# Kernel tuning notes

Hardware: AMD Instinct MI355X
Metric: run time of the kernel (lower is better)

## Reference

```python
import jax, jax.numpy as jnp
import numpy as np

B, S, D, H = 2, 2048, 1024, 16
DK = D // H
WINDOW = 256


def _make_mask():
    # causal local-window sparsity: attend to j in (i-WINDOW, i]
    i = np.arange(S)[:, None]
    j = np.arange(S)[None, :]
    m = (j <= i) & (i - j < WINDOW)
    return jnp.asarray(m)


def setup_inputs() -> dict:
    key = jax.random.key(0)
    ks = jax.random.split(key, 9)
    sw = 1.0 / np.sqrt(D)
    return {
        "x": jax.random.normal(ks[0], (B, S, D), dtype=jnp.float32),
        "wq": jax.random.normal(ks[1], (D, D), dtype=jnp.float32) * sw,
        "bq": jnp.zeros((D,), dtype=jnp.float32),
        "wk": jax.random.normal(ks[2], (D, D), dtype=jnp.float32) * sw,
        "bk": jnp.zeros((D,), dtype=jnp.float32),
        "wv": jax.random.normal(ks[3], (D, D), dtype=jnp.float32) * sw,
        "bv": jnp.zeros((D,), dtype=jnp.float32),
        "wo": jax.random.normal(ks[4], (D, D), dtype=jnp.float32) * sw,
        "bo": jnp.zeros((D,), dtype=jnp.float32),
        "mask": _make_mask(),
    }


def reference(x, wq, bq, wk, bk, wv, bv, wo, bo, mask):
    b, s, d = x.shape
    # projections (torch Linear: x @ W.T + b), split heads -> [b, h, s, dk]
    def proj(w, bias):
        return (x @ w.T + bias).reshape(b, s, H, DK).transpose(0, 2, 1, 3)

    q = proj(wq, bq)
    k = proj(wk, bk)
    v = proj(wv, bv)

    scores = jnp.einsum("bhqd,bhkd->bhqk", q, k) / jnp.sqrt(jnp.float32(DK))
    scores = jnp.where(mask, scores, -jnp.inf)  # mask broadcasts over b, h
    attn = jax.nn.softmax(scores, axis=-1)
    out = jnp.einsum("bhqk,bhkd->bhqd", attn, v)
    out = out.transpose(0, 2, 1, 3).reshape(b, s, d)
    return out @ wo.T + bo
```

## Files before the change

### kernel.cpp

```cpp
#include <hip/hip_runtime.h>

#define S_LEN 2048
#define DMODEL 1024
#define NHEADS 16
#define WIN 256

typedef unsigned short u16;
typedef unsigned int u32;
typedef __attribute__((ext_vector_type(8))) __bf16 bf16x8;
typedef __attribute__((ext_vector_type(4))) float f32x4;
typedef __attribute__((ext_vector_type(8))) u16 u16x8;
typedef __attribute__((ext_vector_type(4))) u16 u16x4;

__device__ __forceinline__ u16 f2bf(float f) {
  u32 u = __builtin_bit_cast(u32, f);
  u += 0x7fffu + ((u >> 16) & 1u);
  return (u16)(u >> 16);
}

#define GLDS16(g, l) __builtin_amdgcn_global_load_lds( \
    (const __attribute__((address_space(1))) void*)(g), \
    (__attribute__((address_space(3))) void*)(l), 16, 0, 0)

__global__ __launch_bounds__(256) void cast_all(
    const float* __restrict__ x, const float* __restrict__ wq, const float* __restrict__ wk,
    const float* __restrict__ wv, const float* __restrict__ wo,
    u16* __restrict__ xb, u16* __restrict__ wqb, u16* __restrict__ wkb,
    u16* __restrict__ wvb, u16* __restrict__ wob) {
  const int e = (blockIdx.x * 256 + threadIdx.x) * 4;
  const float* src; u16* dst; int off;
  if (e < (1 << 22)) { src = x; dst = xb; off = e; }
  else {
    int r = e - (1 << 22);
    int seg = r >> 20; off = r & ((1 << 20) - 1);
    src = (seg == 0) ? wq : (seg == 1) ? wk : (seg == 2) ? wv : wo;
    dst = (seg == 0) ? wqb : (seg == 1) ? wkb : (seg == 2) ? wvb : wob;
  }
  float4 v = *(const float4*)(src + off);
  u16x4 o = { f2bf(v.x), f2bf(v.y), f2bf(v.z), f2bf(v.w) };
  *(u16x4*)(dst + off) = o;
}

__global__ __launch_bounds__(256) void gemm_nt(
    const u16* __restrict__ A,
    const u16* __restrict__ B0, const u16* __restrict__ B1, const u16* __restrict__ B2,
    const float* __restrict__ bias0, const float* __restrict__ bias1, const float* __restrict__ bias2,
    u16* __restrict__ C0, u16* __restrict__ C1, u16* __restrict__ C2,
    const int M, const int N, const int K)
{
  const u16* Bt; const float* bias; u16* C;
  if (blockIdx.z == 0)      { Bt = B0; bias = bias0; C = C0; }
  else if (blockIdx.z == 1) { Bt = B1; bias = bias1; C = C1; }
  else                      { Bt = B2; bias = bias2; C = C2; }

  __shared__ u16 As[2][128 * 32];
  __shared__ u16 Bs[2][128 * 32];

  const int t = threadIdx.x;
  const int row0 = blockIdx.x * 128;
  const int col0 = blockIdx.y * 128;
  const int lane = t & 63, lo = lane & 15, hi = lane >> 4;
  const int wv = t >> 6;
  const int wr = (wv >> 1) * 64, wc = (wv & 1) * 64;

  f32x4 acc[4][4];
  #pragma unroll
  for (int i = 0; i < 4; ++i)
    #pragma unroll
    for (int j = 0; j < 4; ++j) acc[i][j] = (f32x4)0.0f;

  const int NT = K >> 5;

  auto stage = [&](int buf, int kt) {
    const int kof = kt * 32;
    #pragma unroll
    for (int c = 0; c < 2; ++c) {
      const int off = t * 16 + c * 4096;
      const int r = off >> 6;
      const int ke = (off & 63) >> 1;
      GLDS16(A  + (size_t)(row0 + r) * K + (kof + ke), (u16*)As + buf * (128 * 32) + (off >> 1));
      GLDS16(Bt + (size_t)(col0 + r) * K + (kof + ke), (u16*)Bs + buf * (128 * 32) + (off >> 1));
    }
  };

  stage(0, 0);
  int cur = 0;
  for (int kt = 0; kt < NT; ++kt) {
    __syncthreads();
    if (kt + 1 < NT) stage(cur ^ 1, kt + 1);
    bf16x8 af[4], bfr[4];
    #pragma unroll
    for (int mi = 0; mi < 4; ++mi)
      af[mi] = *(const bf16x8*)&As[cur][(wr + mi * 16 + lo) * 32 + hi * 8];
    #pragma unroll
    for (int ni = 0; ni < 4; ++ni)
      bfr[ni] = *(const bf16x8*)&Bs[cur][(wc + ni * 16 + lo) * 32 + hi * 8];
    #pragma unroll
    for (int mi = 0; mi < 4; ++mi)
      #pragma unroll
      for (int ni = 0; ni < 4; ++ni)
        acc[mi][ni] = __builtin_amdgcn_mfma_f32_16x16x32_bf16(af[mi], bfr[ni], acc[mi][ni], 0, 0, 0);
    cur ^= 1;
  }

  #pragma unroll
  for (int mi = 0; mi < 4; ++mi) {
    #pragma unroll
    for (int ni = 0; ni < 4; ++ni) {
      const int col = col0 + wc + ni * 16 + lo;
      const float bv = bias[col];
      #pragma unroll
      for (int r = 0; r < 4; ++r) {
        const int row = row0 + wr + mi * 16 + hi * 4 + r;
        C[(size_t)row * N + col] = f2bf(acc[mi][ni][r] + bv);
      }
    }
  }
}

__global__ __launch_bounds__(256) void gemm_out64(
    const u16* __restrict__ A, const u16* __restrict__ Bt,
    const float* __restrict__ bias, float* __restrict__ C)
{
  constexpr int N = 1024, K = 1024;

  __shared__ u16 As[2][128 * 32];
  __shared__ u16 Bs[2][64 * 32];

  int id = blockIdx.y * gridDim.x + blockIdx.x;
  int wgid = (id & 7) * 64 + (id >> 3);
  const int row0 = (wgid >> 4) * 128;
  const int col0 = (wgid & 15) * 64;

  const int t = threadIdx.x;
  const int lane = t & 63, lo = lane & 15, hi = lane >> 4;
  const int wv = t >> 6;
  const int wr = (wv >> 1) * 64, wc = (wv & 1) * 32;

  f32x4 acc[4][2];
  #pragma unroll
  for (int i = 0; i < 4; ++i)
    #pragma unroll
    for (int j = 0; j < 2; ++j) acc[i][j] = (f32x4)0.0f;

  auto stage = [&](int buf, int kt) {
    const int kof = kt * 32;
    #pragma unroll
    for (int c = 0; c < 2; ++c) {
      const int off = t * 16 + c * 4096;
      const int r = off >> 6;
      const int ke = (off & 63) >> 1;
      GLDS16(A + (size_t)(row0 + r) * K + (kof + ke), (u16*)As + buf * (128 * 32) + (off >> 1));
    }
    {
      const int off = t * 16;
      const int r = off >> 6;
      const int ke = (off & 63) >> 1;
      GLDS16(Bt + (size_t)(col0 + r) * K + (kof + ke), (u16*)Bs + buf * (64 * 32) + (off >> 1));
    }
  };

  stage(0, 0);
  int cur = 0;
  for (int kt = 0; kt < (K >> 5); ++kt) {
    __syncthreads();
    if (kt + 1 < (K >> 5)) stage(cur ^ 1, kt + 1);
    bf16x8 af[4], bfr[2];
    #pragma unroll
    for (int mi = 0; mi < 4; ++mi)
      af[mi] = *(const bf16x8*)&As[cur][(wr + mi * 16 + lo) * 32 + hi * 8];
    #pragma unroll
    for (int ni = 0; ni < 2; ++ni)
      bfr[ni] = *(const bf16x8*)&Bs[cur][(wc + ni * 16 + lo) * 32 + hi * 8];
    #pragma unroll
    for (int mi = 0; mi < 4; ++mi)
      #pragma unroll
      for (int ni = 0; ni < 2; ++ni)
        acc[mi][ni] = __builtin_amdgcn_mfma_f32_16x16x32_bf16(af[mi], bfr[ni], acc[mi][ni], 0, 0, 0);
    cur ^= 1;
  }

  #pragma unroll
  for (int mi = 0; mi < 4; ++mi) {
    #pragma unroll
    for (int ni = 0; ni < 2; ++ni) {
      const int col = col0 + wc + ni * 16 + lo;
      const float bv = bias[col];
      #pragma unroll
      for (int r = 0; r < 4; ++r) {
        const int row = row0 + wr + mi * 16 + hi * 4 + r;
        C[(size_t)row * N + col] = acc[mi][ni][r] + bv;
      }
    }
  }
}

__device__ __forceinline__ int swzK(int row, int col) {
  int byte = (row << 7) + (col << 1);
  byte ^= (row & 7) << 4;
  return byte >> 1;
}
__device__ __forceinline__ int swzV(int d, int j) {
  int byte = (d << 7) + (j << 1);
  byte ^= ((d & 7) << 4) ^ (((d >> 4) & 3) << 5);
  return byte >> 1;
}

__global__ __launch_bounds__(512) void attn_win(const u16* __restrict__ Q,
                                                const u16* __restrict__ K,
                                                const u16* __restrict__ V,
                                                u16* __restrict__ O) {
  const int qt = blockIdx.x, h = blockIdx.y, b = blockIdx.z;
  const int q0 = qt * 128;
  const int t = threadIdx.x;
  const int wv = t >> 6, lane = t & 63, lo = lane & 15, hi = lane >> 4;

  __shared__ u16 Ks[2][64 * 64];
  __shared__ u16 Vt[2][64 * 64];
  __shared__ u16 Ps[8][16 * 64];

  const size_t base = ((size_t)b * S_LEN) * DMODEL + h * 64;
  const int w0 = q0 + wv * 16;

  bf16x8 qf[2];
  {
    const u16* qp = Q + base + (size_t)(w0 + lo) * DMODEL;
    u16x8 qa = *(const u16x8*)(qp + hi * 8);
    u16x8 qb = *(const u16x8*)(qp + 32 + hi * 8);
    union { u16x8 s; bf16x8 v; } ua, ub;
    #pragma unroll
    for (int e = 0; e < 8; ++e) {
      float fa = __builtin_bit_cast(float, (u32)qa[e] << 16) * 0.125f;
      float fb = __builtin_bit_cast(float, (u32)qb[e] << 16) * 0.125f;
      ua.s[e] = (u16)(__builtin_bit_cast(u32, fa) >> 16);
      ub.s[e] = (u16)(__builtin_bit_cast(u32, fb) >> 16);
    }
    qf[0] = ua.v; qf[1] = ub.v;
  }

  const int vrow = t >> 3;
  const int vc0  = (t & 7) * 8;
  const int ktmin = max(0, (256 - q0) >> 6);

  u16x8 kra, vra;
  auto issue = [&](int kt) {
    const int jg = q0 - 256 + kt * 64 + vrow;
    if (jg >= 0) {
      kra = *(const u16x8*)(K + base + (size_t)jg * DMODEL + vc0);
      vra = *(const u16x8*)(V + base + (size_t)jg * DMODEL + vc0);
    } else { kra = (u16x8)0; vra = (u16x8)0; }
  };
  auto commit = [&](int buf) {
    *(u16x8*)&Ks[buf][swzK(vrow, vc0)] = kra;
    #pragma unroll
    for (int e = 0; e < 8; ++e)
      Vt[buf][swzV(vc0 + e, vrow)] = vra[e];
  };

  issue(ktmin);
  commit(0);
  __syncthreads();

  f32x4 oacc[4];
  #pragma unroll
  for (int i = 0; i < 4; ++i) oacc[i] = (f32x4)0.0f;
  float l_r[4] = {0.f, 0.f, 0.f, 0.f};

  int cur = 0;
  for (int kt = ktmin; kt < 6; ++kt) {
    const int kstart = q0 - 256 + kt * 64;
    if (kt < 5) issue(kt + 1);

    const bool act = (kstart <= w0 + 15) && (kstart + 63 >= w0 - 255);
    if (act) {
      f32x4 sfr[4];
      #pragma unroll
      for (int ni = 0; ni < 4; ++ni) {
        sfr[ni] = (f32x4)0.0f;
        #pragma unroll
        for (int kq = 0; kq < 2; ++kq) {
          bf16x8 kf = *(const bf16x8*)&Ks[cur][swzK(ni * 16 + lo, kq * 32 + hi * 8)];
          sfr[ni] = __builtin_amdgcn_mfma_f32_16x16x32_bf16(qf[kq], kf, sfr[ni], 0, 0, 0);
        }
      }

      const int i0 = w0 + hi * 4;
      float pr[4][4];
      #pragma unroll
      for (int ni = 0; ni < 4; ++ni) {
        const int j = kstart + ni * 16 + lo;
        #pragma unroll
        for (int r = 0; r < 4; ++r) {
          const int i = i0 + r;
          const bool ok = (j >= 0) & (j <= i) & (i - j < WIN);
          const float x = ok ? sfr[ni][r] : -1e30f;
          const float p = __expf(x);
          pr[ni][r] = p;
          l_r[r] += p;
        }
      }

      #pragma unroll
      for (int ni = 0; ni < 4; ++ni)
        #pragma unroll
        for (int r = 0; r < 4; ++r)
          Ps[wv][swzK(hi * 4 + r, ni * 16 + lo)] = f2bf(pr[ni][r]);

      bf16x8 pa[2];
      #pragma unroll
      for (int kp = 0; kp < 2; ++kp)
        pa[kp] = *(const bf16x8*)&Ps[wv][swzK(lo, kp * 32 + hi * 8)];

      #pragma unroll
      for (int ni = 0; ni < 4; ++ni) {
        #pragma unroll
        for (int kp = 0; kp < 2; ++kp) {
          bf16x8 vf = *(const bf16x8*)&Vt[cur][swzV(ni * 16 + lo, kp * 32 + hi * 8)];
          oacc[ni] = __builtin_amdgcn_mfma_f32_16x16x32_bf16(pa[kp], vf, oacc[ni], 0, 0, 0);
        }
      }
    }

    if (kt < 5) commit(cur ^ 1);
    __syncthreads();
    cur ^= 1;
  }

  #pragma unroll
  for (int d = 1; d < 16; d <<= 1) {
    #pragma unroll
    for (int r = 0; r < 4; ++r) l_r[r] += __shfl_xor(l_r[r], d);
  }

  #pragma unroll
  for (int r = 0; r < 4; ++r) {
    const float inv = 1.0f / l_r[r];
    const int row = w0 + hi * 4 + r;
    #pragma unroll
    for (int ni = 0; ni < 4; ++ni)
      O[base + (size_t)row * DMODEL + ni * 16 + lo] = f2bf(oacc[ni][r] * inv);
  }
}

extern "C" void kernel_launch(void* const* d_in, const int* in_sizes, int n_in,
                              void* d_out, int out_size, void* d_ws, size_t ws_size,
                              hipStream_t stream) {
  const float* x  = (const float*)d_in[0];
  const float* wq = (const float*)d_in[1];
  const float* bq = (const float*)d_in[2];
  const float* wk = (const float*)d_in[3];
  const float* bk = (const float*)d_in[4];
  const float* wvp = (const float*)d_in[5];
  const float* bv = (const float*)d_in[6];
  const float* wo = (const float*)d_in[7];
  const float* bo = (const float*)d_in[8];
  float* out = (float*)d_out;

  char* ws = (char*)d_ws;
  const size_t MB = 1024 * 1024;
  u16* xb  = (u16*)(ws);
  u16* wqb = (u16*)(ws + 8 * MB);
  u16* wkb = (u16*)(ws + 10 * MB);
  u16* wvb = (u16*)(ws + 12 * MB);
  u16* wob = (u16*)(ws + 14 * MB);
  u16* Qb  = (u16*)(ws + 16 * MB);
  u16* Kb  = (u16*)(ws + 24 * MB);
  u16* Vb  = (u16*)(ws + 32 * MB);
  u16* Ob  = (u16*)(ws + 40 * MB);

  cast_all<<<8192, 256, 0, stream>>>(x, wq, wk, wvp, wo, xb, wqb, wkb, wvb, wob);

  dim3 g1(4096 / 128, 1024 / 128, 3);
  gemm_nt<<<g1, 256, 0, stream>>>(xb, wqb, wkb, wvb, bq, bk, bv,
                                  Qb, Kb, Vb, 4096, 1024, 1024);

  attn_win<<<dim3(S_LEN / 128, NHEADS, 2), 512, 0, stream>>>(Qb, Kb, Vb, Ob);

  gemm_out64<<<dim3(32, 16), 256, 0, stream>>>(Ob, wob, bo, out);
}
```

Before: 85.43 us.

## Rewrite QKV projection GEMM as 256x256 tile, 8-wave phased pipeline

Replaces the 128x128 QKV GEMM (256 threads, K-step 32) with a 256x256 tile kernel using 8 waves, K-step 64, XOR-swizzled LDS to avoid bank conflicts, and a four-phase schedule. Within each phase LDS reads, global-to-LDS prefetches and MFMA groups are interleaved, gated by explicit vmcnt/lgkmcnt waits, barriers and setprio. The intent is more data reuse per tile and overlap of memory traffic with matrix math. The trade-off is a grid of only 192 blocks, which may underfill the device, plus heavy register and LDS use.

```diff
diff --git a/kernel.cpp b/kernel.cpp
--- a/kernel.cpp
+++ b/kernel.cpp
@@ -21,6 +21,10 @@
 #define GLDS16(g, l) __builtin_amdgcn_global_load_lds( \
     (const __attribute__((address_space(1))) void*)(g), \
     (__attribute__((address_space(3))) void*)(l), 16, 0, 0)
+
+#define BAR() { asm volatile("" ::: "memory"); __builtin_amdgcn_s_barrier(); asm volatile("" ::: "memory"); }
+#define LGKM0() { asm volatile("s_waitcnt lgkmcnt(0)" ::: "memory"); __builtin_amdgcn_sched_barrier(0); }
+#define VMCNT(n) asm volatile("s_waitcnt vmcnt(" #n ")" ::: "memory")
 
 __global__ __launch_bounds__(256) void cast_all(
     const float* __restrict__ x, const float* __restrict__ wq, const float* __restrict__ wk,
@@ -41,78 +45,145 @@
   *(u16x4*)(dst + off) = o;
 }
 
-__global__ __launch_bounds__(256) void gemm_nt(
+__global__ __launch_bounds__(512, 2) void gemm_qkv_8ph(
     const u16* __restrict__ A,
-    const u16* __restrict__ B0, const u16* __restrict__ B1, const u16* __restrict__ B2,
-    const float* __restrict__ bias0, const float* __restrict__ bias1, const float* __restrict__ bias2,
-    u16* __restrict__ C0, u16* __restrict__ C1, u16* __restrict__ C2,
-    const int M, const int N, const int K)
+    const u16* __restrict__ Wq, const u16* __restrict__ Wk, const u16* __restrict__ Wv,
+    const float* __restrict__ bq, const float* __restrict__ bk, const float* __restrict__ bv,
+    u16* __restrict__ Qo, u16* __restrict__ Ko, u16* __restrict__ Vo)
 {
-  const u16* Bt; const float* bias; u16* C;
-  if (blockIdx.z == 0)      { Bt = B0; bias = bias0; C = C0; }
-  else if (blockIdx.z == 1) { Bt = B1; bias = bias1; C = C1; }
-  else                      { Bt = B2; bias = bias2; C = C2; }
-
-  __shared__ u16 As[2][128 * 32];
-  __shared__ u16 Bs[2][128 * 32];
+  constexpr int K = 1024, NT = 16;
+
+  __shared__ u16 AS[2][2][8192];
+  __shared__ u16 BS[2][2][8192];
 
   const int t = threadIdx.x;
-  const int row0 = blockIdx.x * 128;
-  const int col0 = blockIdx.y * 128;
   const int lane = t & 63, lo = lane & 15, hi = lane >> 4;
-  const int wv = t >> 6;
-  const int wr = (wv >> 1) * 64, wc = (wv & 1) * 64;
-
-  f32x4 acc[4][4];
-  #pragma unroll
-  for (int i = 0; i < 4; ++i)
+  const int wid = t >> 6, wm = wid >> 2, wn = wid & 3;
+  const int sx = lo & 7;
+
+  const int row0 = blockIdx.x * 256;
+  const int by = blockIdx.y;
+  const int wsel = by >> 2;
+  const int col0 = (by & 3) * 256;
+  const u16* Bt = (wsel == 0) ? Wq : (wsel == 1) ? Wk : Wv;
+  const float* bias = (wsel == 0) ? bq : (wsel == 1) ? bk : bv;
+  u16* C = (wsel == 0) ? Qo : (wsel == 1) ? Ko : Vo;
+
+  const int srow = t >> 3;
+  const int kcol = (t & 7) ^ ((t >> 3) & 7);
+
+  auto stageA = [&](int slot, int kt, int h) {
+    #pragma unroll
+    for (int c = 0; c < 2; ++c)
+      GLDS16(A + (size_t)(row0 + h * 128 + c * 64 + srow) * K + kt * 64 + kcol * 8,
+             (u16*)AS + slot * 16384 + h * 8192 + c * 4096 + t * 8);
+  };
+  auto stageB = [&](int slot, int kt, int h) {
+    #pragma unroll
+    for (int c = 0; c < 2; ++c)
+      GLDS16(Bt + (size_t)(col0 + h * 128 + c * 64 + srow) * K + kt * 64 + kcol * 8,
+             (u16*)BS + slot * 16384 + h * 8192 + c * 4096 + t * 8);
+  };
+  auto rdA = [&](int slot, int m, int kk) -> bf16x8 {
+    const int byte = ((m * 16 + lo) << 7) + ((((kk << 2) + hi) ^ sx) << 4);
+    return *(const bf16x8*)((const char*)AS + slot * 32768 + wm * 16384 + byte);
+  };
+  auto rdB = [&](int slot, int n, int kk) -> bf16x8 {
+    const int byte = (((wn & 1) * 64 + n * 16 + lo) << 7) + ((((kk << 2) + hi) ^ sx) << 4);
+    return *(const bf16x8*)((const char*)BS + slot * 32768 + (wn >> 1) * 16384 + byte);
+  };
+
+  f32x4 acc[8][4];
+  #pragma unroll
+  for (int i = 0; i < 8; ++i)
     #pragma unroll
     for (int j = 0; j < 4; ++j) acc[i][j] = (f32x4)0.0f;
 
-  const int NT = K >> 5;
-
-  auto stage = [&](int buf, int kt) {
-    const int kof = kt * 32;
-    #pragma unroll
-    for (int c = 0; c < 2; ++c) {
-      const int off = t * 16 + c * 4096;
-      const int r = off >> 6;
-      const int ke = (off & 63) >> 1;
-      GLDS16(A  + (size_t)(row0 + r) * K + (kof + ke), (u16*)As + buf * (128 * 32) + (off >> 1));
-      GLDS16(Bt + (size_t)(col0 + r) * K + (kof + ke), (u16*)Bs + buf * (128 * 32) + (off >> 1));
-    }
-  };
-
-  stage(0, 0);
-  int cur = 0;
-  for (int kt = 0; kt < NT; ++kt) {
-    __syncthreads();
-    if (kt + 1 < NT) stage(cur ^ 1, kt + 1);
-    bf16x8 af[4], bfr[4];
-    #pragma unroll
-    for (int mi = 0; mi < 4; ++mi)
-      af[mi] = *(const bf16x8*)&As[cur][(wr + mi * 16 + lo) * 32 + hi * 8];
-    #pragma unroll
-    for (int ni = 0; ni < 4; ++ni)
-      bfr[ni] = *(const bf16x8*)&Bs[cur][(wc + ni * 16 + lo) * 32 + hi * 8];
-    #pragma unroll
-    for (int mi = 0; mi < 4; ++mi)
-      #pragma unroll
-      for (int ni = 0; ni < 4; ++ni)
-        acc[mi][ni] = __builtin_amdgcn_mfma_f32_16x16x32_bf16(af[mi], bfr[ni], acc[mi][ni], 0, 0, 0);
-    cur ^= 1;
-  }
-
-  #pragma unroll
-  for (int mi = 0; mi < 4; ++mi) {
-    #pragma unroll
-    for (int ni = 0; ni < 4; ++ni) {
-      const int col = col0 + wc + ni * 16 + lo;
-      const float bv = bias[col];
+  bf16x8 a[4][2], b0[2][2], b1[2][2];
+
+  stageA(0, 0, 0); stageA(0, 0, 1); stageB(0, 0, 0); stageB(0, 0, 1);
+  stageA(1, 1, 0); stageA(1, 1, 1);
+  VMCNT(4);
+  BAR();
+
+  for (int u = 0; u < NT; ++u) {
+    const int slot = u & 1;
+    const bool nx1 = (u + 1 < NT), nx2 = (u + 2 < NT);
+
+    #pragma unroll
+    for (int m = 0; m < 4; ++m) { a[m][0] = rdA(slot, m, 0); a[m][1] = rdA(slot, m, 1); }
+    #pragma unroll
+    for (int n = 0; n < 2; ++n) { b0[n][0] = rdB(slot, n, 0); b0[n][1] = rdB(slot, n, 1); }
+    if (nx1) stageB(slot ^ 1, u + 1, 0);
+    BAR();
+    LGKM0();
+    __builtin_amdgcn_s_setprio(1);
+    #pragma unroll
+    for (int m = 0; m < 4; ++m)
+      #pragma unroll
+      for (int n = 0; n < 2; ++n)
+        #pragma unroll
+        for (int kk = 0; kk < 2; ++kk)
+          acc[m][n] = __builtin_amdgcn_mfma_f32_16x16x32_bf16(a[m][kk], b0[n][kk], acc[m][n], 0, 0, 0);
+    __builtin_amdgcn_s_setprio(0);
+    BAR();
+
+    #pragma unroll
+    for (int n = 0; n < 2; ++n) { b1[n][0] = rdB(slot, 2 + n, 0); b1[n][1] = rdB(slot, 2 + n, 1); }
+    if (nx1) stageB(slot ^ 1, u + 1, 1);
+    BAR();
+    LGKM0();
+    __builtin_amdgcn_s_setprio(1);
+    #pragma unroll
+    for (int m = 0; m < 4; ++m)
+      #pragma unroll
+      for (int n = 0; n < 2; ++n)
+        #pragma unroll
+        for (int kk = 0; kk < 2; ++kk)
+          acc[m][2 + n] = __builtin_amdgcn_mfma_f32_16x16x32_bf16(a[m][kk], b1[n][kk], acc[m][2 + n], 0, 0, 0);
+    __builtin_amdgcn_s_setprio(0);
+    BAR();
+
+    #pragma unroll
+    for (int m = 0; m < 4; ++m) { a[m][0] = rdA(slot, 4 + m, 0); a[m][1] = rdA(slot, 4 + m, 1); }
+    BAR();
+    LGKM0();
+    __builtin_amdgcn_s_setprio(1);
+    #pragma unroll
+    for (int m = 0; m < 4; ++m)
+      #pragma unroll
+      for (int n = 0; n < 2; ++n)
+        #pragma unroll
+        for (int kk = 0; kk < 2; ++kk)
+          acc[4 + m][2 + n] = __builtin_amdgcn_mfma_f32_16x16x32_bf16(a[m][kk], b1[n][kk], acc[4 + m][2 + n], 0, 0, 0);
+    __builtin_amdgcn_s_setprio(0);
+    BAR();
+
+    if (nx2) { stageA(slot, u + 2, 0); stageA(slot, u + 2, 1); }
+    if (nx2) { VMCNT(4); } else { VMCNT(0); }
+    BAR();
+    __builtin_amdgcn_s_setprio(1);
+    #pragma unroll
+    for (int m = 0; m < 4; ++m)
+      #pragma unroll
+      for (int n = 0; n < 2; ++n)
+        #pragma unroll
+        for (int kk = 0; kk < 2; ++kk)
+          acc[4 + m][n] = __builtin_amdgcn_mfma_f32_16x16x32_bf16(a[m][kk], b0[n][kk], acc[4 + m][n], 0, 0, 0);
+    __builtin_amdgcn_s_setprio(0);
+    BAR();
+  }
+
+  #pragma unroll
+  for (int m = 0; m < 8; ++m) {
+    #pragma unroll
+    for (int n = 0; n < 4; ++n) {
+      const int col = col0 + wn * 64 + n * 16 + lo;
+      const float bb = bias[col];
       #pragma unroll
       for (int r = 0; r < 4; ++r) {
-        const int row = row0 + wr + mi * 16 + hi * 4 + r;
-        C[(size_t)row * N + col] = f2bf(acc[mi][ni][r] + bv);
+        const int row = row0 + wm * 128 + m * 16 + hi * 4 + r;
+        C[(size_t)row * DMODEL + col] = f2bf(acc[m][n][r] + bb);
       }
     }
   }
@@ -370,9 +441,7 @@
 
   cast_all<<<8192, 256, 0, stream>>>(x, wq, wk, wvp, wo, xb, wqb, wkb, wvb, wob);
 
-  dim3 g1(4096 / 128, 1024 / 128, 3);
-  gemm_nt<<<g1, 256, 0, stream>>>(xb, wqb, wkb, wvb, bq, bk, bv,
-                                  Qb, Kb, Vb, 4096, 1024, 1024);
+  gemm_qkv_8ph<<<dim3(16, 12), 512, 0, stream>>>(xb, wqb, wkb, wvb, bq, bk, bv, Qb, Kb, Vb);
 
   attn_win<<<dim3(S_LEN / 128, NHEADS, 2), 512, 0, stream>>>(Qb, Kb, Vb, Ob);
 
```

New measurement: 87.76 us. 2.7% more time.

## Swizzle GEMM LDS tiles and prefetch two stages ahead with vmcnt waits

Applied to the files above, without the earlier changes.

Both GEMM kernels now XOR-swizzle the 16-byte k-groups by row when staging into LDS. The fragment reads use the matching XOR index, which is meant to remove LDS bank conflicts on the bf16x8 loads. The pipeline now issues two stages up front and prefetches tile kt+2. Each iteration waits with an explicit s_waitcnt vmcnt count and a raw barrier instead of __syncthreads, so global loads can stay in flight across iterations. The hand-set vmcnt counts depend on the exact number of loads per stage, and a second barrier is added per iteration.

```diff
diff --git a/kernel.cpp b/kernel.cpp
--- a/kernel.cpp
+++ b/kernel.cpp
@@ -21,6 +21,9 @@
 #define GLDS16(g, l) __builtin_amdgcn_global_load_lds( \
     (const __attribute__((address_space(1))) void*)(g), \
     (__attribute__((address_space(3))) void*)(l), 16, 0, 0)
+
+#define BAR() { asm volatile("" ::: "memory"); __builtin_amdgcn_s_barrier(); asm volatile("" ::: "memory"); }
+#define VMCNT(n) asm volatile("s_waitcnt vmcnt(" #n ")" ::: "memory")
 
 __global__ __launch_bounds__(256) void cast_all(
     const float* __restrict__ x, const float* __restrict__ wq, const float* __restrict__ wk,
@@ -62,6 +65,7 @@
   const int lane = t & 63, lo = lane & 15, hi = lane >> 4;
   const int wv = t >> 6;
   const int wr = (wv >> 1) * 64, wc = (wv & 1) * 64;
+  const int sx = lo & 3;
 
   f32x4 acc[4][4];
   #pragma unroll
@@ -77,30 +81,36 @@
     for (int c = 0; c < 2; ++c) {
       const int off = t * 16 + c * 4096;
       const int r = off >> 6;
-      const int ke = (off & 63) >> 1;
-      GLDS16(A  + (size_t)(row0 + r) * K + (kof + ke), (u16*)As + buf * (128 * 32) + (off >> 1));
-      GLDS16(Bt + (size_t)(col0 + r) * K + (kof + ke), (u16*)Bs + buf * (128 * 32) + (off >> 1));
+      const int g = ((off >> 4) & 3) ^ (r & 3);
+      GLDS16(A  + (size_t)(row0 + r) * K + (kof + g * 8), (u16*)As + buf * 4096 + (off >> 1));
+      GLDS16(Bt + (size_t)(col0 + r) * K + (kof + g * 8), (u16*)Bs + buf * 4096 + (off >> 1));
     }
   };
 
   stage(0, 0);
-  int cur = 0;
+  stage(1, 1);
   for (int kt = 0; kt < NT; ++kt) {
-    __syncthreads();
-    if (kt + 1 < NT) stage(cur ^ 1, kt + 1);
+    const int cur = kt & 1;
+    if (kt + 1 < NT) { VMCNT(4); } else { VMCNT(0); }
+    BAR();
     bf16x8 af[4], bfr[4];
     #pragma unroll
-    for (int mi = 0; mi < 4; ++mi)
-      af[mi] = *(const bf16x8*)&As[cur][(wr + mi * 16 + lo) * 32 + hi * 8];
-    #pragma unroll
-    for (int ni = 0; ni < 4; ++ni)
-      bfr[ni] = *(const bf16x8*)&Bs[cur][(wc + ni * 16 + lo) * 32 + hi * 8];
+    for (int mi = 0; mi < 4; ++mi) {
+      const int row = wr + mi * 16 + lo;
+      af[mi] = *(const bf16x8*)&As[cur][row * 32 + ((hi ^ sx) << 3)];
+    }
+    #pragma unroll
+    for (int ni = 0; ni < 4; ++ni) {
+      const int row = wc + ni * 16 + lo;
+      bfr[ni] = *(const bf16x8*)&Bs[cur][row * 32 + ((hi ^ sx) << 3)];
+    }
     #pragma unroll
     for (int mi = 0; mi < 4; ++mi)
       #pragma unroll
       for (int ni = 0; ni < 4; ++ni)
         acc[mi][ni] = __builtin_amdgcn_mfma_f32_16x16x32_bf16(af[mi], bfr[ni], acc[mi][ni], 0, 0, 0);
-    cur ^= 1;
+    BAR();
+    if (kt + 2 < NT) stage(cur, kt + 2);
   }
 
   #pragma unroll
@@ -136,6 +146,7 @@
   const int lane = t & 63, lo = lane & 15, hi = lane >> 4;
   const int wv = t >> 6;
   const int wr = (wv >> 1) * 64, wc = (wv & 1) * 32;
+  const int sx = lo & 3;
 
   f32x4 acc[4][2];
   #pragma unroll
@@ -149,35 +160,41 @@
     for (int c = 0; c < 2; ++c) {
       const int off = t * 16 + c * 4096;
       const int r = off >> 6;
-      const int ke = (off & 63) >> 1;
-      GLDS16(A + (size_t)(row0 + r) * K + (kof + ke), (u16*)As + buf * (128 * 32) + (off >> 1));
+      const int g = ((off >> 4) & 3) ^ (r & 3);
+      GLDS16(A + (size_t)(row0 + r) * K + (kof + g * 8), (u16*)As + buf * 4096 + (off >> 1));
     }
     {
       const int off = t * 16;
       const int r = off >> 6;
-      const int ke = (off & 63) >> 1;
-      GLDS16(Bt + (size_t)(col0 + r) * K + (kof + ke), (u16*)Bs + buf * (64 * 32) + (off >> 1));
+      const int g = ((off >> 4) & 3) ^ (r & 3);
+      GLDS16(Bt + (size_t)(col0 + r) * K + (kof + g * 8), (u16*)Bs + buf * 2048 + (off >> 1));
     }
   };
 
   stage(0, 0);
-  int cur = 0;
+  stage(1, 1);
   for (int kt = 0; kt < (K >> 5); ++kt) {
-    __syncthreads();
-    if (kt + 1 < (K >> 5)) stage(cur ^ 1, kt + 1);
+    const int cur = kt & 1;
+    if (kt + 1 < (K >> 5)) { VMCNT(3); } else { VMCNT(0); }
+    BAR();
     bf16x8 af[4], bfr[2];
     #pragma unroll
-    for (int mi = 0; mi < 4; ++mi)
-      af[mi] = *(const bf16x8*)&As[cur][(wr + mi * 16 + lo) * 32 + hi * 8];
-    #pragma unroll
-    for (int ni = 0; ni < 2; ++ni)
-      bfr[ni] = *(const bf16x8*)&Bs[cur][(wc + ni * 16 + lo) * 32 + hi * 8];
+    for (int mi = 0; mi < 4; ++mi) {
+      const int row = wr + mi * 16 + lo;
+      af[mi] = *(const bf16x8*)&As[cur][row * 32 + ((hi ^ sx) << 3)];
+    }
+    #pragma unroll
+    for (int ni = 0; ni < 2; ++ni) {
+      const int row = wc + ni * 16 + lo;
+      bfr[ni] = *(const bf16x8*)&Bs[cur][row * 32 + ((hi ^ sx) << 3)];
+    }
     #pragma unroll
     for (int mi = 0; mi < 4; ++mi)
       #pragma unroll
       for (int ni = 0; ni < 2; ++ni)
         acc[mi][ni] = __builtin_amdgcn_mfma_f32_16x16x32_bf16(af[mi], bfr[ni], acc[mi][ni], 0, 0, 0);
-    cur ^= 1;
+    BAR();
+    if (kt + 2 < (K >> 5)) stage(cur, kt + 2);
   }
 
   #pragma unroll
```

After: 81.43 us. 4.7% less time.
